# Kernel tuning notes

Measured on AMD Instinct MI355X. Metric: run time of the kernel, lower is better.

The kernel has to match this reference:

```python
import jax, jax.numpy as jnp
import numpy as np

N, K = 8192, 64          # num pixels (b*h*w), proj_dim
C, M = 19, 10            # num_classes, num_prototype


def setup_inputs() -> dict:
    key = jax.random.key(0)
    k1, k2, k3 = jax.random.split(key, 3)
    x = jax.random.normal(k1, (N, K), dtype=jnp.float32)
    x_var = jax.random.uniform(k2, (N, K), dtype=jnp.float32)  # positive variances
    proto_mean = jax.random.normal(k3, (C, M, K), dtype=jnp.float32) * 0.02  # trunc_normal std=0.02
    proto_var = jnp.ones((C, M, K), dtype=jnp.float32)
    return {"x": x, "x_var": x_var, "proto_mean": proto_mean, "proto_var": proto_var}


def reference(x, x_var, proto_mean, proto_var):
    # MLS similarity: sim = -0.5 * mean_k[ (mu - x)^2 / (sig_x + sig_p) + log(sig_x + sig_p) ]
    pm = proto_mean[:, :, None, :]            # (c, m, 1, k)
    pv = proto_var[:, :, None, :]             # (c, m, 1, k)
    mean_diff = jnp.square(pm - x)            # (c, m, n, k) broadcast
    var_sum = x_var + pv                      # (c, m, n, k)
    sim = mean_diff / var_sum + jnp.log(var_sum)
    sim = -0.5 * jnp.mean(sim, axis=-1)       # (c, m, n)
    return jnp.transpose(sim, (2, 0, 1))      # (n, c, m) == permute(2, 0, 1)
```

## Files before the change

kernel.cpp:

```cpp
#include <hip/hip_runtime.h>

#define NROWS 8192
#define KDIM 64
#define CDIM 19
#define MDIM 10
#define CMDIM (CDIM * MDIM)
#define CM_PER_BLOCK 19
#define ROWS_PER_BLOCK 64
#define LDS_STRIDE 65

__global__ __launch_bounds__(256)
void probproto_kernel(const float* __restrict__ x,
                      const float* __restrict__ xv,
                      const float* __restrict__ pm,
                      const float* __restrict__ pv,
                      float* __restrict__ out)
{
    __shared__ float xs_t[KDIM * LDS_STRIDE];
    __shared__ float xvs_t[KDIM * LDS_STRIDE];
    __shared__ float pms[CM_PER_BLOCK * KDIM];
    __shared__ float pvs[CM_PER_BLOCK * KDIM];

    const int t   = threadIdx.x;
    const int n0  = blockIdx.x * ROWS_PER_BLOCK;
    const int cm0 = blockIdx.y * CM_PER_BLOCK;

    const float4* x4  = (const float4*)(x  + (size_t)n0 * KDIM);
    const float4* xv4 = (const float4*)(xv + (size_t)n0 * KDIM);
    #pragma unroll
    for (int i = 0; i < 4; ++i) {
        int idx = t + 256 * i;
        int r   = idx >> 4;
        int c4  = idx & 15;
        float4 a = x4[idx];
        float4 b = xv4[idx];
        int k = c4 * 4;
        xs_t[(k + 0) * LDS_STRIDE + r] = a.x;
        xs_t[(k + 1) * LDS_STRIDE + r] = a.y;
        xs_t[(k + 2) * LDS_STRIDE + r] = a.z;
        xs_t[(k + 3) * LDS_STRIDE + r] = a.w;
        xvs_t[(k + 0) * LDS_STRIDE + r] = b.x;
        xvs_t[(k + 1) * LDS_STRIDE + r] = b.y;
        xvs_t[(k + 2) * LDS_STRIDE + r] = b.z;
        xvs_t[(k + 3) * LDS_STRIDE + r] = b.w;
    }
    for (int idx = t; idx < CM_PER_BLOCK * KDIM; idx += 256) {
        pms[idx] = pm[cm0 * KDIM + idx];
        pvs[idx] = pv[cm0 * KDIM + idx];
    }
    __syncthreads();

    const int wave = t >> 6;
    const int lane = t & 63;
    const int n    = n0 + lane;

    for (int cmi = wave; cmi < CM_PER_BLOCK; cmi += 4) {
        float accQ = 0.0f;
        float accL = 0.0f;
        for (int kc = 0; kc < 4; ++kc) {
            float prod = 1.0f;
            #pragma unroll
            for (int k8 = 0; k8 < 16; ++k8) {
                int k = kc * 16 + k8;
                float pmv = pms[cmi * KDIM + k];
                float pvv = pvs[cmi * KDIM + k];
                float xx  = xs_t[k * LDS_STRIDE + lane];
                float xvv = xvs_t[k * LDS_STRIDE + lane];
                float v = xvv + pvv;
                float d = pmv - xx;
                accQ = fmaf(d * d, __builtin_amdgcn_rcpf(v), accQ);
                prod *= v;
            }
            accL += __log2f(prod);
        }
        out[(size_t)n * CMDIM + cm0 + cmi] =
            -(accQ + 0.69314718055994531f * accL) * (1.0f / 128.0f);
    }
}

extern "C" void kernel_launch(void* const* d_in, const int* in_sizes, int n_in,
                              void* d_out, int out_size, void* d_ws, size_t ws_size,
                              hipStream_t stream) {
    const float* x  = (const float*)d_in[0];
    const float* xv = (const float*)d_in[1];
    const float* pm = (const float*)d_in[2];
    const float* pv = (const float*)d_in[3];
    float* out = (float*)d_out;

    dim3 grid(NROWS / ROWS_PER_BLOCK, CMDIM / CM_PER_BLOCK);
    probproto_kernel<<<grid, 256, 0, stream>>>(x, xv, pm, pv, out);
}
```

Before: 83.83 us.

## Load prototypes via scalar float4 reads and reuse x registers across prototypes

Drops the LDS staging of prototype mean/variance. Prototype values are now read straight from global memory as wave-uniform float4 loads, which can go through scalar loads because the wave index is made uniform with readfirstlane. The loop is reordered so each 16-wide k chunk of x and x_var is read from LDS into registers once and reused across the up to five prototypes a wave handles. This cuts LDS traffic and removes the prototype staging loop, at the cost of more registers for the accumulators and x chunks.

New measurement: 90.38 us. 7.8% more time.

```diff
diff --git a/kernel.cpp b/kernel.cpp
--- a/kernel.cpp
+++ b/kernel.cpp
@@ -18,8 +18,6 @@
 {
     __shared__ float xs_t[KDIM * LDS_STRIDE];
     __shared__ float xvs_t[KDIM * LDS_STRIDE];
-    __shared__ float pms[CM_PER_BLOCK * KDIM];
-    __shared__ float pvs[CM_PER_BLOCK * KDIM];
 
     const int t   = threadIdx.x;
     const int n0  = blockIdx.x * ROWS_PER_BLOCK;
@@ -44,37 +42,59 @@
         xvs_t[(k + 2) * LDS_STRIDE + r] = b.z;
         xvs_t[(k + 3) * LDS_STRIDE + r] = b.w;
     }
-    for (int idx = t; idx < CM_PER_BLOCK * KDIM; idx += 256) {
-        pms[idx] = pm[cm0 * KDIM + idx];
-        pvs[idx] = pv[cm0 * KDIM + idx];
-    }
     __syncthreads();
 
-    const int wave = t >> 6;
+    const int wave = __builtin_amdgcn_readfirstlane(t >> 6);
     const int lane = t & 63;
     const int n    = n0 + lane;
 
-    for (int cmi = wave; cmi < CM_PER_BLOCK; cmi += 4) {
-        float accQ = 0.0f;
-        float accL = 0.0f;
-        for (int kc = 0; kc < 4; ++kc) {
-            float prod = 1.0f;
-            #pragma unroll
-            for (int k8 = 0; k8 < 16; ++k8) {
-                int k = kc * 16 + k8;
-                float pmv = pms[cmi * KDIM + k];
-                float pvv = pvs[cmi * KDIM + k];
-                float xx  = xs_t[k * LDS_STRIDE + lane];
-                float xvv = xvs_t[k * LDS_STRIDE + lane];
-                float v = xvv + pvv;
-                float d = pmv - xx;
-                accQ = fmaf(d * d, __builtin_amdgcn_rcpf(v), accQ);
-                prod *= v;
+    const float4* __restrict__ pm4 = (const float4*)(pm + (size_t)cm0 * KDIM);
+    const float4* __restrict__ pv4 = (const float4*)(pv + (size_t)cm0 * KDIM);
+
+    float accQ[5] = {0.f, 0.f, 0.f, 0.f, 0.f};
+    float accL[5] = {0.f, 0.f, 0.f, 0.f, 0.f};
+
+    #pragma unroll
+    for (int kc = 0; kc < 4; ++kc) {
+        float xr[16], xvr[16];
+        #pragma unroll
+        for (int i = 0; i < 16; ++i) {
+            xr[i]  = xs_t [(kc * 16 + i) * LDS_STRIDE + lane];
+            xvr[i] = xvs_t[(kc * 16 + i) * LDS_STRIDE + lane];
+        }
+        #pragma unroll
+        for (int j = 0; j < 5; ++j) {
+            const int cmi = wave + 4 * j;
+            if (cmi < CM_PER_BLOCK) {
+                float q    = accQ[j];
+                float prod = 1.0f;
+                #pragma unroll
+                for (int i4 = 0; i4 < 4; ++i4) {
+                    const float4 pmv = pm4[cmi * 16 + kc * 4 + i4];
+                    const float4 pvv = pv4[cmi * 16 + kc * 4 + i4];
+                    float v, d;
+                    v = xvr[i4 * 4 + 0] + pvv.x;  d = pmv.x - xr[i4 * 4 + 0];
+                    q = fmaf(d * d, __builtin_amdgcn_rcpf(v), q);  prod *= v;
+                    v = xvr[i4 * 4 + 1] + pvv.y;  d = pmv.y - xr[i4 * 4 + 1];
+                    q = fmaf(d * d, __builtin_amdgcn_rcpf(v), q);  prod *= v;
+                    v = xvr[i4 * 4 + 2] + pvv.z;  d = pmv.z - xr[i4 * 4 + 2];
+                    q = fmaf(d * d, __builtin_amdgcn_rcpf(v), q);  prod *= v;
+                    v = xvr[i4 * 4 + 3] + pvv.w;  d = pmv.w - xr[i4 * 4 + 3];
+                    q = fmaf(d * d, __builtin_amdgcn_rcpf(v), q);  prod *= v;
+                }
+                accQ[j] = q;
+                accL[j] += __log2f(prod);
             }
-            accL += __log2f(prod);
         }
-        out[(size_t)n * CMDIM + cm0 + cmi] =
-            -(accQ + 0.69314718055994531f * accL) * (1.0f / 128.0f);
+    }
+
+    #pragma unroll
+    for (int j = 0; j < 5; ++j) {
+        const int cmi = wave + 4 * j;
+        if (cmi < CM_PER_BLOCK) {
+            out[(size_t)n * CMDIM + cm0 + cmi] =
+                -(accQ[j] + 0.69314718055994531f * accL[j]) * (1.0f / 128.0f);
+        }
     }
 }
 
```
